# Performance work log

Measured on AMD Instinct MI355X. Metric: run time of the kernel, lower is better.

The kernel has to match this reference:

```python
import jax, jax.numpy as jnp
import numpy as np

RES = (32, 32, 32)   # S, H, W
WS = 4               # window size (cubic)
SHIFT = 2            # shift size
NH = 6               # num heads
C = 192              # dim
EPS = 1e-5


def _rel_pos_index(ws):
    coords = np.stack(np.meshgrid(np.arange(ws), np.arange(ws), np.arange(ws), indexing='ij'))
    cf = coords.reshape(3, -1)                      # (3, N)
    rc = (cf[:, :, None] - cf[:, None, :]).transpose(1, 2, 0).astype(np.int64)  # (N,N,3)
    rc[..., 0] += ws - 1
    rc[..., 1] += ws - 1
    rc[..., 2] += ws - 1
    rc[..., 0] *= 3 * ws - 1
    rc[..., 1] *= 2 * ws - 1
    return rc.sum(-1)                               # (N, N)

_RPI = jnp.asarray(_rel_pos_index(WS))


def _ln(x, g, b):
    m = jnp.mean(x, axis=-1, keepdims=True)
    v = jnp.mean(jnp.square(x - m), axis=-1, keepdims=True)
    return (x - m) * jax.lax.rsqrt(v + EPS) * g + b


def setup_inputs():
    key = jax.random.key(0)
    ks = jax.random.split(key, 12)
    B, L = 2, RES[0] * RES[1] * RES[2]
    nW, N = 512, WS ** 3
    Hd = 4 * C
    p = lambda k, s: jax.random.normal(k, s, jnp.float32) * 0.02
    return {
        'x': jax.random.normal(ks[0], (B, L, C), jnp.float32),
        'mask_matrix': jax.random.normal(ks[1], (nW, N, N), jnp.float32),
        'skip': jax.random.normal(ks[2], (B, L, C), jnp.float32),
        'x_up': jax.random.normal(ks[3], (B, L, C), jnp.float32),
        'norm1_g': jnp.ones((C,), jnp.float32), 'norm1_b': jnp.zeros((C,), jnp.float32),
        'kv_w': p(ks[4], (C, 2 * C)), 'kv_b': jnp.zeros((2 * C,), jnp.float32),
        'rpb_table': p(ks[5], ((2 * WS - 1) ** 3, NH)),
        'proj_w': p(ks[6], (C, C)), 'proj_b': jnp.zeros((C,), jnp.float32),
        'norm2_g': jnp.ones((C,), jnp.float32), 'norm2_b': jnp.zeros((C,), jnp.float32),
        'fc1_w': p(ks[7], (C, Hd)), 'fc1_b': jnp.zeros((Hd,), jnp.float32),
        'fc2_w': p(ks[8], (Hd, C)), 'fc2_b': jnp.zeros((C,), jnp.float32),
    }


def reference(x, mask_matrix, skip, x_up, norm1_g, norm1_b, kv_w, kv_b, rpb_table,
              proj_w, proj_b, norm2_g, norm2_b, fc1_w, fc1_b, fc2_w, fc2_b):
    B, L, _ = x.shape
    S, H, W = RES
    ws, N = WS, WS ** 3
    hd = C // NH
    scale = hd ** -0.5

    sn = _ln(skip, norm1_g, norm1_b).reshape(B, S, H, W, C)
    qn = _ln(x_up, norm1_g, norm1_b).reshape(B, S, H, W, C)
    # cyclic shift (shift_size > 0)
    sn = jnp.roll(sn, (-SHIFT, -SHIFT, -SHIFT), axis=(1, 2, 3))
    qn = jnp.roll(qn, (-SHIFT, -SHIFT, -SHIFT), axis=(1, 2, 3))

    def part(t):  # window partition -> (B*nW, N, C)
        t = t.reshape(B, S // ws, ws, H // ws, ws, W // ws, ws, C)
        return t.transpose(0, 1, 3, 5, 2, 4, 6, 7).reshape(-1, N, C)

    skw, qw = part(sn), part(qn)
    B_ = skw.shape[0]

    kv = (skw @ kv_w + kv_b).reshape(B_, N, 2, NH, hd)
    k = kv[:, :, 0].transpose(0, 2, 1, 3)   # (B_, NH, N, hd)
    v = kv[:, :, 1].transpose(0, 2, 1, 3)
    q = qw.reshape(B_, N, NH, hd).transpose(0, 2, 1, 3) * scale

    attn = jnp.einsum('bhqd,bhkd->bhqk', q, k)
    rpb = rpb_table[_RPI.reshape(-1)].reshape(N, N, NH).transpose(2, 0, 1)  # (NH, N, N)
    attn = attn + rpb[None]
    nW = mask_matrix.shape[0]
    attn = attn.reshape(B, nW, NH, N, N) + mask_matrix[None, :, None]
    attn = jax.nn.softmax(attn.reshape(B_, NH, N, N), axis=-1)

    out = jnp.einsum('bhqk,bhkd->bhqd', attn, v).transpose(0, 2, 1, 3).reshape(B_, N, C)
    out = out @ proj_w + proj_b

    # window reverse
    out = out.reshape(B, S // ws, H // ws, W // ws, ws, ws, ws, C)
    out = out.transpose(0, 1, 4, 2, 5, 3, 6, 7).reshape(B, S, H, W, C)
    out = jnp.roll(out, (SHIFT, SHIFT, SHIFT), axis=(1, 2, 3)).reshape(B, L, C)

    x = x + out
    h = _ln(x, norm2_g, norm2_b)
    h = jax.nn.gelu(h @ fc1_w + fc1_b, approximate=False) @ fc2_w + fc2_b
    return x + h
```

## Files before the change

### kernel.cpp

```cpp
#include <hip/hip_runtime.h>
#include <math.h>

typedef unsigned short u16;
typedef __bf16 bf16x8 __attribute__((ext_vector_type(8)));
typedef float f32x4 __attribute__((ext_vector_type(4)));
typedef unsigned short u16x8 __attribute__((ext_vector_type(8)));

#define SHIFT 2

static __device__ __forceinline__ f32x4 mfma16(bf16x8 a, bf16x8 b, f32x4 c) {
  return __builtin_amdgcn_mfma_f32_16x16x32_bf16(a, b, c, 0, 0, 0);
}
static __device__ __forceinline__ u16 f2bf(float f) {
  unsigned u = __builtin_bit_cast(unsigned, f);
  unsigned r = u + 0x7fffu + ((u >> 16) & 1u);
  return (u16)(r >> 16);
}
static __device__ __forceinline__ float bf2f(u16 u) {
  unsigned v = (unsigned)u << 16;
  return __builtin_bit_cast(float, v);
}
static __device__ __forceinline__ void stage16(const u16* g, u16* lbase, int lane) {
#if __has_builtin(__builtin_amdgcn_global_load_lds)
  __builtin_amdgcn_global_load_lds(
      (const __attribute__((address_space(1))) unsigned int*)g,
      (__attribute__((address_space(3))) unsigned int*)lbase, 16, 0, 0);
#else
  *(u16x8*)(lbase + lane * 8) = *(const u16x8*)g;
#endif
}

#define OFF_KVWT  ((size_t)0)
#define OFF_PRWT  (OFF_KVWT + 384*192*2)
#define OFF_FC1WT (OFF_PRWT + 192*192*2)
#define OFF_FC2WT (OFF_FC1WT + 768*192*2)
#define OFF_SKW   (OFF_FC2WT + 192*768*2)
#define OFF_QW    (OFF_SKW + (size_t)65536*192*2)
#define OFF_KVB   (OFF_QW + (size_t)65536*192*2)
#define OFF_POX   (OFF_KVB + (size_t)65536*384*2)
#define OFF_YB    (OFF_POX + (size_t)65536*192*2)
#define OFF_HN    (OFF_YB + (size_t)65536*192*2)
#define OFF_RPBG  (OFF_HN + (size_t)65536*192*2)

__global__ __launch_bounds__(256) void k_prep(
    const float* __restrict__ kv_w, const float* __restrict__ proj_w,
    const float* __restrict__ fc1_w, const float* __restrict__ fc2_w,
    const float* __restrict__ rpb,
    u16* __restrict__ kvT, u16* __restrict__ prT,
    u16* __restrict__ f1T, u16* __restrict__ f2T, u16* __restrict__ rpbg) {
  int i = blockIdx.x * 256 + threadIdx.x;
  if (i < 192 * 384) kvT[(i % 384) * 192 + i / 384] = f2bf(kv_w[i]);
  if (i < 192 * 192) prT[(i % 192) * 192 + i / 192] = f2bf(proj_w[i]);
  if (i < 192 * 768) f1T[(i % 768) * 192 + i / 768] = f2bf(fc1_w[i]);
  if (i < 768 * 192) f2T[(i % 192) * 768 + i / 192] = f2bf(fc2_w[i]);
  if (i < 24576) {
    int h = i >> 12, rem = i & 4095, qr = rem >> 6, kc = rem & 63;
    int qs = qr >> 4, qh = (qr >> 2) & 3, qx = qr & 3;
    int ks = kc >> 4, kh = (kc >> 2) & 3, kx = kc & 3;
    int idx = (qs - ks + 3) * 11 + (qh - kh + 3) * 7 + (qx - kx + 3);
    rpbg[i] = f2bf(rpb[idx * 6 + h]);
  }
}

__global__ __launch_bounds__(256) void k_ln_part(
    const float* __restrict__ skip, const float* __restrict__ x_up,
    const float* __restrict__ gam, const float* __restrict__ bet,
    u16* __restrict__ skw, u16* __restrict__ qw) {
  int row = blockIdx.x * 4 + (threadIdx.x >> 6);
  int lane = threadIdx.x & 63;
  const float* sp = skip + (size_t)row * 192;
  const float* qp = x_up + (size_t)row * 192;
  float sv[3], qv[3], ss = 0.f, qs = 0.f;
#pragma unroll
  for (int j = 0; j < 3; j++) {
    sv[j] = sp[lane + 64 * j]; qv[j] = qp[lane + 64 * j];
    ss += sv[j]; qs += qv[j];
  }
#pragma unroll
  for (int m = 1; m < 64; m <<= 1) { ss += __shfl_xor(ss, m, 64); qs += __shfl_xor(qs, m, 64); }
  float sm = ss * (1.f / 192.f), qm = qs * (1.f / 192.f);
  float s2 = 0.f, q2 = 0.f;
#pragma unroll
  for (int j = 0; j < 3; j++) { float d = sv[j] - sm; s2 += d * d; d = qv[j] - qm; q2 += d * d; }
#pragma unroll
  for (int m = 1; m < 64; m <<= 1) { s2 += __shfl_xor(s2, m, 64); q2 += __shfl_xor(q2, m, 64); }
  float sr = rsqrtf(s2 * (1.f / 192.f) + 1e-5f), qr = rsqrtf(q2 * (1.f / 192.f) + 1e-5f);
  int b = row >> 15, l = row & 32767;
  int s = l >> 10, h = (l >> 5) & 31, w = l & 31;
  int s_ = (s - SHIFT) & 31, h_ = (h - SHIFT) & 31, w_ = (w - SHIFT) & 31;
  int wIdx = ((s_ >> 2) * 8 + (h_ >> 2)) * 8 + (w_ >> 2);
  int n = ((s_ & 3) * 4 + (h_ & 3)) * 4 + (w_ & 3);
  size_t orow = ((size_t)(b * 512 + wIdx) * 64 + n) * 192;
  const float scale = 0.17677669529663687f;
#pragma unroll
  for (int j = 0; j < 3; j++) {
    int cc = lane + 64 * j;
    float gg = gam[cc], bb = bet[cc];
    skw[orow + cc] = f2bf((sv[j] - sm) * sr * gg + bb);
    qw[orow + cc]  = f2bf(((qv[j] - qm) * qr * gg + bb) * scale);
  }
}

__global__ __launch_bounds__(256, 2) void k_kv(
    const u16* __restrict__ A, const u16* __restrict__ BT,
    const float* __restrict__ bias, u16* __restrict__ outh) {
  __shared__ u16 lw[192 * 192];
  int mb = blockIdx.x, nb = blockIdx.y;
  int tid = threadIdx.x, l = tid & 63, wv = tid >> 6, g = l >> 4, c = l & 15;
  int wr = wv >> 1, wc = wv & 1;
#pragma unroll
  for (int i = 0; i < 18; i++) {
    int CI = i * 256 + tid;
    int row = CI / 24, ch = CI % 24;
    int sch = (ch & 24) | ((ch ^ row) & 7);
    stage16(BT + (size_t)(nb * 192 + row) * 192 + sch * 8, lw + (i * 256 + wv * 64) * 8, l);
  }
  __syncthreads();
  f32x4 acc[4][6] = {};
#pragma unroll
  for (int ks = 0; ks < 6; ks++) {
    bf16x8 a[4];
#pragma unroll
    for (int m = 0; m < 4; m++)
      a[m] = *(const bf16x8*)&A[(size_t)(mb * 128 + wr * 64 + m * 16 + c) * 192 + ks * 32 + g * 8];
#pragma unroll
    for (int n = 0; n < 6; n++) {
      int col = wc * 96 + n * 16 + c;
      int ch = ks * 4 + g;
      int chp = (ch & 24) | ((ch ^ col) & 7);
      bf16x8 b = *(const bf16x8*)&lw[col * 192 + chp * 8];
#pragma unroll
      for (int m = 0; m < 4; m++) acc[m][n] = mfma16(a[m], b, acc[m][n]);
    }
  }
#pragma unroll
  for (int n = 0; n < 6; n++)
#pragma unroll
    for (int m = 0; m < 4; m++) {
      int col = nb * 192 + wc * 96 + n * 16 + c;
      float bb = bias[col];
#pragma unroll
      for (int r = 0; r < 4; r++) {
        int row = mb * 128 + wr * 64 + m * 16 + g * 4 + r;
        outh[(size_t)row * 384 + col] = f2bf(acc[m][n][r] + bb);
      }
    }
}

__global__ __launch_bounds__(384) void k_attn_mega(
    const u16* __restrict__ qw, const u16* __restrict__ kvb,
    const u16* __restrict__ rpbg, const float* __restrict__ mask,
    const u16* __restrict__ prT, const float* __restrict__ proj_b,
    u16* __restrict__ pox) {
  __shared__ __align__(16) char smem[38400];
  u16* lv = (u16*)smem;
  u16* lo = (u16*)smem;
  u16* lp = (u16*)(smem + 24576);
  int b_ = blockIdx.x, wIdx = b_ & 511;
  int tid = threadIdx.x, l = tid & 63, wv = tid >> 6, g = l >> 4, c = l & 15;
  int h = wv;
#pragma unroll
  for (int i = 0; i < 4; i++) {
    int CI = i * 384 + tid;
    int row = CI / 24, ch = CI % 24;
    stage16(kvb + ((size_t)b_ * 64 + row) * 384 + 192 + ch * 8,
            lv + (i * 384 + wv * 64) * 8, l);
  }
  const float* mrow = mask + (size_t)wIdx * 4096;
  float4 mv[4][4];
#pragma unroll
  for (int n = 0; n < 4; n++)
#pragma unroll
    for (int m = 0; m < 4; m++)
      mv[n][m] = *(const float4*)&mrow[(n * 16 + c) * 64 + m * 16 + g * 4];
  bf16x8 qa[4], kb[4];
#pragma unroll
  for (int m = 0; m < 4; m++)
    qa[m] = *(const bf16x8*)&qw[((size_t)b_ * 64 + m * 16 + c) * 192 + h * 32 + g * 8];
#pragma unroll
  for (int n = 0; n < 4; n++)
    kb[n] = *(const bf16x8*)&kvb[((size_t)b_ * 64 + n * 16 + c) * 384 + h * 32 + g * 8];
  __syncthreads();
  bf16x8 vb[2][2];
#pragma unroll
  for (int kk = 0; kk < 2; kk++)
#pragma unroll
    for (int nd = 0; nd < 2; nd++) {
      union { u16 u[8]; bf16x8 v; } bb;
#pragma unroll
      for (int j = 0; j < 8; j++)
        bb.u[j] = lv[(kk * 32 + g * 8 + j) * 192 + h * 32 + nd * 16 + c];
      vb[kk][nd] = bb.v;
    }
  __syncthreads();
  f32x4 acc[4][4] = {};
#pragma unroll
  for (int m = 0; m < 4; m++)
#pragma unroll
    for (int n = 0; n < 4; n++) acc[m][n] = mfma16(kb[m], qa[n], acc[m][n]);
  const u16* rg = rpbg + h * 4096;
  f32x4 oacc[4][2] = {};
#pragma unroll
  for (int n = 0; n < 4; n++) {
    ushort4 rv[4];
#pragma unroll
    for (int m = 0; m < 4; m++)
      rv[m] = *(const ushort4*)&rg[(n * 16 + c) * 64 + m * 16 + g * 4];
    float vals[4][4];
    float mx = -3.4e38f;
#pragma unroll
    for (int m = 0; m < 4; m++) {
      float mr[4] = {mv[n][m].x, mv[n][m].y, mv[n][m].z, mv[n][m].w};
      u16 ru[4] = {rv[m].x, rv[m].y, rv[m].z, rv[m].w};
#pragma unroll
      for (int r = 0; r < 4; r++) {
        vals[m][r] = acc[m][n][r] + bf2f(ru[r]) + mr[r];
        mx = fmaxf(mx, vals[m][r]);
      }
    }
    mx = fmaxf(mx, __shfl_xor(mx, 16, 64));
    mx = fmaxf(mx, __shfl_xor(mx, 32, 64));
    float sum = 0.f;
#pragma unroll
    for (int m = 0; m < 4; m++)
#pragma unroll
      for (int r = 0; r < 4; r++) { vals[m][r] = __expf(vals[m][r] - mx); sum += vals[m][r]; }
    sum += __shfl_xor(sum, 16, 64);
    sum += __shfl_xor(sum, 32, 64);
    float inv = 1.f / sum;
#pragma unroll
    for (int m = 0; m < 4; m++) {
      unsigned p0 = f2bf(vals[m][0] * inv) | ((unsigned)f2bf(vals[m][1] * inv) << 16);
      unsigned p1 = f2bf(vals[m][2] * inv) | ((unsigned)f2bf(vals[m][3] * inv) << 16);
      *(uint2*)&lp[h * 1152 + c * 72 + m * 16 + g * 4] = make_uint2(p0, p1);
    }
#pragma unroll
    for (int kk = 0; kk < 2; kk++) {
      bf16x8 pa = *(const bf16x8*)&lp[h * 1152 + c * 72 + kk * 32 + g * 8];
#pragma unroll
      for (int nd = 0; nd < 2; nd++) oacc[n][nd] = mfma16(pa, vb[kk][nd], oacc[n][nd]);
    }
  }
  __syncthreads();
#pragma unroll
  for (int m = 0; m < 4; m++)
#pragma unroll
    for (int nd = 0; nd < 2; nd++)
#pragma unroll
      for (int r = 0; r < 4; r++)
        lo[(m * 16 + g * 4 + r) * 200 + h * 32 + nd * 16 + c] = f2bf(oacc[m][nd][r]);
  __syncthreads();
  f32x4 pacc[4][2] = {};
#pragma unroll
  for (int ks = 0; ks < 6; ks++) {
    bf16x8 pa[4];
#pragma unroll
    for (int m = 0; m < 4; m++)
      pa[m] = *(const bf16x8*)&lo[(m * 16 + c) * 200 + ks * 32 + g * 8];
#pragma unroll
    for (int n = 0; n < 2; n++) {
      bf16x8 pb = *(const bf16x8*)&prT[(size_t)(wv * 32 + n * 16 + c) * 192 + ks * 32 + g * 8];
#pragma unroll
      for (int m = 0; m < 4; m++) pacc[m][n] = mfma16(pa[m], pb, pacc[m][n]);
    }
  }
#pragma unroll
  for (int m = 0; m < 4; m++)
#pragma unroll
    for (int r = 0; r < 4; r++) {
      int tok = m * 16 + g * 4 + r;
#pragma unroll
      for (int n = 0; n < 2; n++) {
        int col = wv * 32 + n * 16 + c;
        pox[((size_t)b_ * 64 + tok) * 192 + col] = f2bf(pacc[m][n][r] + proj_b[col]);
      }
    }
}

__global__ __launch_bounds__(256) void k_ln2(
    const float* __restrict__ x, const u16* __restrict__ pox,
    const float* __restrict__ g2, const float* __restrict__ b2,
    u16* __restrict__ yb, u16* __restrict__ hn) {
  int row = blockIdx.x * 4 + (threadIdx.x >> 6);
  int lane = threadIdx.x & 63;
  int b = row >> 15, ll = row & 32767;
  int s = ll >> 10, hh = (ll >> 5) & 31, w = ll & 31;
  int s_ = (s - SHIFT) & 31, h_ = (hh - SHIFT) & 31, w_ = (w - SHIFT) & 31;
  int wI = ((s_ >> 2) * 8 + (h_ >> 2)) * 8 + (w_ >> 2);
  int n = ((s_ & 3) * 4 + (h_ & 3)) * 4 + (w_ & 3);
  size_t wrow = ((size_t)(b * 512 + wI) * 64 + n) * 192;
  float y[3]; float ss = 0.f, sq = 0.f;
#pragma unroll
  for (int j = 0; j < 3; j++) {
    int cc = lane + 64 * j;
    y[j] = x[(size_t)row * 192 + cc] + bf2f(pox[wrow + cc]);
    ss += y[j]; sq += y[j] * y[j];
  }
#pragma unroll
  for (int m = 1; m < 64; m <<= 1) { ss += __shfl_xor(ss, m, 64); sq += __shfl_xor(sq, m, 64); }
  float mu = ss * (1.f / 192.f);
  float rs = rsqrtf(sq * (1.f / 192.f) - mu * mu + 1e-5f);
#pragma unroll
  for (int j = 0; j < 3; j++) {
    int cc = lane + 64 * j;
    yb[(size_t)row * 192 + cc] = f2bf(y[j]);
    hn[(size_t)row * 192 + cc] = f2bf((y[j] - mu) * rs * g2[cc] + b2[cc]);
  }
}

__global__ __launch_bounds__(256) void k_mlp(
    const u16* __restrict__ hn, const u16* __restrict__ f1T,
    const u16* __restrict__ f2T, const float* __restrict__ b1,
    const float* __restrict__ b2f, const u16* __restrict__ yb,
    float* __restrict__ out) {
  __shared__ u16 lds[29184];
  u16* f1c = lds;
  u16* f2c = lds + 12288;
  u16* h1c = lds + 24576;
  int tid = threadIdx.x, l = tid & 63, wv = tid >> 6, g = l >> 4, c = l & 15;
  size_t tokbase = (size_t)blockIdx.x * 64;
#pragma unroll
  for (int i = 0; i < 6; i++) {
    int CI = i * 256 + wv * 64 + l;
    int row = CI / 24, chp = CI % 24;
    int sch = (chp & 24) | ((chp ^ row) & 7);
    stage16(hn + (tokbase + row) * 192 + sch * 8, f1c + (i * 256 + wv * 64) * 8, l);
  }
  __syncthreads();
  bf16x8 hb[4][6];
#pragma unroll
  for (int tf = 0; tf < 4; tf++)
#pragma unroll
    for (int ks = 0; ks < 6; ks++) {
      int ch = ks * 4 + g;
      int chp = (ch & 24) | ((ch ^ c) & 7);
      hb[tf][ks] = *(const bf16x8*)&f1c[(tf * 16 + c) * 192 + chp * 8];
    }
  f32x4 acc2[3][4] = {};
#pragma unroll 1
  for (int ko = 0; ko < 12; ko++) {
    __syncthreads();
#pragma unroll
    for (int i = 0; i < 6; i++) {
      int CI = i * 256 + wv * 64 + l;
      int row = CI / 24, chp = CI % 24;
      int sch = (chp & 24) | ((chp ^ row) & 7);
      stage16(f1T + (size_t)(ko * 64 + row) * 192 + sch * 8,
              f1c + (i * 256 + wv * 64) * 8, l);
    }
#pragma unroll
    for (int i = 0; i < 6; i++) {
      int CI = i * 256 + wv * 64 + l;
      int row = CI >> 3, chp = CI & 7;
      int sch = chp ^ (row & 7);
      stage16(f2T + (size_t)row * 768 + ko * 64 + sch * 8,
              f2c + (i * 256 + wv * 64) * 8, l);
    }
    __syncthreads();
    f32x4 acc1[4] = {};
#pragma unroll
    for (int ks = 0; ks < 6; ks++) {
      int ch = ks * 4 + g;
      int chp = (ch & 24) | ((ch ^ c) & 7);
      bf16x8 wa = *(const bf16x8*)&f1c[(wv * 16 + c) * 192 + chp * 8];
#pragma unroll
      for (int tf = 0; tf < 4; tf++) acc1[tf] = mfma16(wa, hb[tf][ks], acc1[tf]);
    }
    float4 b1v = *(const float4*)&b1[ko * 64 + wv * 16 + g * 4];
#pragma unroll
    for (int tf = 0; tf < 4; tf++) {
      unsigned pk[2];
#pragma unroll
      for (int p = 0; p < 2; p++) {
        unsigned lohi[2];
#pragma unroll
        for (int q = 0; q < 2; q++) {
          int r = p * 2 + q;
          float v = acc1[tf][r] + (r == 0 ? b1v.x : r == 1 ? b1v.y : r == 2 ? b1v.z : b1v.w);
          float u2 = v * (1.5957691216f + 0.0713548163f * v * v);
          v = v * (1.f / (1.f + __expf(-u2)));
          lohi[q] = f2bf(v);
        }
        pk[p] = lohi[0] | (lohi[1] << 16);
      }
      *(uint2*)&h1c[(tf * 16 + c) * 72 + wv * 16 + g * 4] = make_uint2(pk[0], pk[1]);
    }
    __syncthreads();
#pragma unroll
    for (int ck = 0; ck < 2; ck++) {
      bf16x8 a2[4];
#pragma unroll
      for (int tf = 0; tf < 4; tf++)
        a2[tf] = *(const bf16x8*)&h1c[(tf * 16 + c) * 72 + ck * 32 + g * 8];
#pragma unroll
      for (int of = 0; of < 3; of++) {
        int ch = ck * 4 + g;
        int chp = ch ^ (c & 7);
        bf16x8 wb = *(const bf16x8*)&f2c[(wv * 48 + of * 16 + c) * 64 + chp * 8];
#pragma unroll
        for (int tf = 0; tf < 4; tf++) acc2[of][tf] = mfma16(a2[tf], wb, acc2[of][tf]);
      }
    }
  }
#pragma unroll
  for (int of = 0; of < 3; of++)
#pragma unroll
    for (int tf = 0; tf < 4; tf++) {
      int col = wv * 48 + of * 16 + c;
      float bb = b2f[col];
#pragma unroll
      for (int r = 0; r < 4; r++) {
        size_t tok = tokbase + tf * 16 + g * 4 + r;
        size_t base = tok * 192 + col;
        out[base] = acc2[of][tf][r] + bb + bf2f(yb[base]);
      }
    }
}

extern "C" void kernel_launch(void* const* d_in, const int* in_sizes, int n_in,
                              void* d_out, int out_size, void* d_ws, size_t ws_size,
                              hipStream_t stream) {
  const float* x      = (const float*)d_in[0];
  const float* mask   = (const float*)d_in[1];
  const float* skip   = (const float*)d_in[2];
  const float* x_up   = (const float*)d_in[3];
  const float* n1g    = (const float*)d_in[4];
  const float* n1b    = (const float*)d_in[5];
  const float* kv_w   = (const float*)d_in[6];
  const float* kv_b   = (const float*)d_in[7];
  const float* rpb    = (const float*)d_in[8];
  const float* proj_w = (const float*)d_in[9];
  const float* proj_b = (const float*)d_in[10];
  const float* n2g    = (const float*)d_in[11];
  const float* n2b    = (const float*)d_in[12];
  const float* fc1_w  = (const float*)d_in[13];
  const float* fc1_b  = (const float*)d_in[14];
  const float* fc2_w  = (const float*)d_in[15];
  const float* fc2_b  = (const float*)d_in[16];
  char* ws = (char*)d_ws;
  u16* kvT  = (u16*)(ws + OFF_KVWT);
  u16* prT  = (u16*)(ws + OFF_PRWT);
  u16* f1T  = (u16*)(ws + OFF_FC1WT);
  u16* f2T  = (u16*)(ws + OFF_FC2WT);
  u16* skw  = (u16*)(ws + OFF_SKW);
  u16* qw   = (u16*)(ws + OFF_QW);
  u16* kvb  = (u16*)(ws + OFF_KVB);
  u16* pox  = (u16*)(ws + OFF_POX);
  u16* yb   = (u16*)(ws + OFF_YB);
  u16* hn   = (u16*)(ws + OFF_HN);
  u16* rpbg = (u16*)(ws + OFF_RPBG);
  float* out = (float*)d_out;

  k_prep<<<dim3(576), dim3(256), 0, stream>>>(kv_w, proj_w, fc1_w, fc2_w, rpb,
                                              kvT, prT, f1T, f2T, rpbg);
  k_ln_part<<<dim3(16384), dim3(256), 0, stream>>>(skip, x_up, n1g, n1b, skw, qw);
  k_kv<<<dim3(512, 2), dim3(256), 0, stream>>>(skw, kvT, kv_b, kvb);
  k_attn_mega<<<dim3(1024), dim3(384), 0, stream>>>(
      qw, kvb, rpbg, mask, prT, proj_b, pox);
  k_ln2<<<dim3(16384), dim3(256), 0, stream>>>(x, pox, n2g, n2b, yb, hn);
  k_mlp<<<dim3(1024), dim3(256), 0, stream>>>(
      hn, f1T, f2T, fc1_b, fc2_b, yb, out);
}
```

Baseline: 223.3 us.

## Repartition MLP kernel so each wave owns 16 tokens and prefetch weights early

The fused MLP kernel now has each wave own 16 tokens across all hidden and output columns, rather than splitting hidden and output columns across waves. Each wave loads its token activations straight from global into registers, and its GELU hidden tile stays in a private LDS region. The fc1 and fc2 weight chunks for the next iteration are staged right after the barrier that frees them, so loads overlap the other GEMM. This aims to cut barrier stalls and expose load latency, but costs more accumulator registers (12 output fragments) and more LDS weight reads per MFMA.

```diff
diff --git a/kernel.cpp b/kernel.cpp
--- a/kernel.cpp
+++ b/kernel.cpp
@@ -318,57 +318,44 @@
   u16* f2c = lds + 12288;
   u16* h1c = lds + 24576;
   int tid = threadIdx.x, l = tid & 63, wv = tid >> 6, g = l >> 4, c = l & 15;
-  size_t tokbase = (size_t)blockIdx.x * 64;
+  size_t tok0 = (size_t)blockIdx.x * 64 + wv * 16;
+  u16* tile = h1c + wv * 1152;
+  bf16x8 hb[6];
+#pragma unroll
+  for (int ks = 0; ks < 6; ks++)
+    hb[ks] = *(const bf16x8*)&hn[(tok0 + c) * 192 + ks * 32 + g * 8];
 #pragma unroll
   for (int i = 0; i < 6; i++) {
-    int CI = i * 256 + wv * 64 + l;
-    int row = CI / 24, chp = CI % 24;
-    int sch = (chp & 24) | ((chp ^ row) & 7);
-    stage16(hn + (tokbase + row) * 192 + sch * 8, f1c + (i * 256 + wv * 64) * 8, l);
-  }
-  __syncthreads();
-  bf16x8 hb[4][6];
-#pragma unroll
-  for (int tf = 0; tf < 4; tf++)
+    int CI = i * 256 + tid;
+    int row = CI / 24, chs = CI % 24;
+    int sch = (chs & 24) | ((chs ^ row) & 7);
+    stage16(f1T + (size_t)row * 192 + sch * 8, f1c + (i * 256 + wv * 64) * 8, l);
+  }
+#pragma unroll
+  for (int i = 0; i < 6; i++) {
+    int CI = i * 256 + tid;
+    int row = CI >> 3, chs = CI & 7;
+    int sch = chs ^ (row & 7);
+    stage16(f2T + (size_t)row * 768 + sch * 8, f2c + (i * 256 + wv * 64) * 8, l);
+  }
+  __syncthreads();
+  f32x4 acc2[12] = {};
+#pragma unroll 1
+  for (int ko = 0; ko < 12; ko++) {
+    f32x4 acc1[4] = {};
 #pragma unroll
     for (int ks = 0; ks < 6; ks++) {
       int ch = ks * 4 + g;
       int chp = (ch & 24) | ((ch ^ c) & 7);
-      hb[tf][ks] = *(const bf16x8*)&f1c[(tf * 16 + c) * 192 + chp * 8];
-    }
-  f32x4 acc2[3][4] = {};
-#pragma unroll 1
-  for (int ko = 0; ko < 12; ko++) {
-    __syncthreads();
-#pragma unroll
-    for (int i = 0; i < 6; i++) {
-      int CI = i * 256 + wv * 64 + l;
-      int row = CI / 24, chp = CI % 24;
-      int sch = (chp & 24) | ((chp ^ row) & 7);
-      stage16(f1T + (size_t)(ko * 64 + row) * 192 + sch * 8,
-              f1c + (i * 256 + wv * 64) * 8, l);
-    }
-#pragma unroll
-    for (int i = 0; i < 6; i++) {
-      int CI = i * 256 + wv * 64 + l;
-      int row = CI >> 3, chp = CI & 7;
-      int sch = chp ^ (row & 7);
-      stage16(f2T + (size_t)row * 768 + ko * 64 + sch * 8,
-              f2c + (i * 256 + wv * 64) * 8, l);
-    }
-    __syncthreads();
-    f32x4 acc1[4] = {};
-#pragma unroll
-    for (int ks = 0; ks < 6; ks++) {
-      int ch = ks * 4 + g;
-      int chp = (ch & 24) | ((ch ^ c) & 7);
-      bf16x8 wa = *(const bf16x8*)&f1c[(wv * 16 + c) * 192 + chp * 8];
-#pragma unroll
-      for (int tf = 0; tf < 4; tf++) acc1[tf] = mfma16(wa, hb[tf][ks], acc1[tf]);
-    }
-    float4 b1v = *(const float4*)&b1[ko * 64 + wv * 16 + g * 4];
-#pragma unroll
-    for (int tf = 0; tf < 4; tf++) {
+#pragma unroll
+      for (int cf = 0; cf < 4; cf++) {
+        bf16x8 wa = *(const bf16x8*)&f1c[(cf * 16 + c) * 192 + chp * 8];
+        acc1[cf] = mfma16(wa, hb[ks], acc1[cf]);
+      }
+    }
+#pragma unroll
+    for (int cf = 0; cf < 4; cf++) {
+      float4 b1v = *(const float4*)&b1[ko * 64 + cf * 16 + g * 4];
       unsigned pk[2];
 #pragma unroll
       for (int p = 0; p < 2; p++) {
@@ -376,45 +363,60 @@
 #pragma unroll
         for (int q = 0; q < 2; q++) {
           int r = p * 2 + q;
-          float v = acc1[tf][r] + (r == 0 ? b1v.x : r == 1 ? b1v.y : r == 2 ? b1v.z : b1v.w);
+          float v = acc1[cf][r] + (r == 0 ? b1v.x : r == 1 ? b1v.y : r == 2 ? b1v.z : b1v.w);
           float u2 = v * (1.5957691216f + 0.0713548163f * v * v);
           v = v * (1.f / (1.f + __expf(-u2)));
           lohi[q] = f2bf(v);
         }
         pk[p] = lohi[0] | (lohi[1] << 16);
       }
-      *(uint2*)&h1c[(tf * 16 + c) * 72 + wv * 16 + g * 4] = make_uint2(pk[0], pk[1]);
+      *(uint2*)&tile[c * 72 + cf * 16 + g * 4] = make_uint2(pk[0], pk[1]);
     }
     __syncthreads();
+    if (ko < 11) {
+#pragma unroll
+      for (int i = 0; i < 6; i++) {
+        int CI = i * 256 + tid;
+        int row = CI / 24, chs = CI % 24;
+        int sch = (chs & 24) | ((chs ^ row) & 7);
+        stage16(f1T + (size_t)((ko + 1) * 64 + row) * 192 + sch * 8,
+                f1c + (i * 256 + wv * 64) * 8, l);
+      }
+    }
 #pragma unroll
     for (int ck = 0; ck < 2; ck++) {
-      bf16x8 a2[4];
-#pragma unroll
-      for (int tf = 0; tf < 4; tf++)
-        a2[tf] = *(const bf16x8*)&h1c[(tf * 16 + c) * 72 + ck * 32 + g * 8];
-#pragma unroll
-      for (int of = 0; of < 3; of++) {
-        int ch = ck * 4 + g;
-        int chp = ch ^ (c & 7);
-        bf16x8 wb = *(const bf16x8*)&f2c[(wv * 48 + of * 16 + c) * 64 + chp * 8];
-#pragma unroll
-        for (int tf = 0; tf < 4; tf++) acc2[of][tf] = mfma16(a2[tf], wb, acc2[of][tf]);
-      }
-    }
-  }
-#pragma unroll
-  for (int of = 0; of < 3; of++)
-#pragma unroll
-    for (int tf = 0; tf < 4; tf++) {
-      int col = wv * 48 + of * 16 + c;
-      float bb = b2f[col];
-#pragma unroll
-      for (int r = 0; r < 4; r++) {
-        size_t tok = tokbase + tf * 16 + g * 4 + r;
-        size_t base = tok * 192 + col;
-        out[base] = acc2[of][tf][r] + bb + bf2f(yb[base]);
-      }
-    }
+      bf16x8 a2 = *(const bf16x8*)&tile[c * 72 + ck * 32 + g * 8];
+      int ch = ck * 4 + g;
+      int chp = ch ^ (c & 7);
+#pragma unroll
+      for (int of = 0; of < 12; of++) {
+        bf16x8 wb = *(const bf16x8*)&f2c[(of * 16 + c) * 64 + chp * 8];
+        acc2[of] = mfma16(a2, wb, acc2[of]);
+      }
+    }
+    __syncthreads();
+    if (ko < 11) {
+#pragma unroll
+      for (int i = 0; i < 6; i++) {
+        int CI = i * 256 + tid;
+        int row = CI >> 3, chs = CI & 7;
+        int sch = chs ^ (row & 7);
+        stage16(f2T + (size_t)row * 768 + (ko + 1) * 64 + sch * 8,
+                f2c + (i * 256 + wv * 64) * 8, l);
+      }
+    }
+  }
+#pragma unroll
+  for (int of = 0; of < 12; of++) {
+    int col = of * 16 + c;
+    float bb = b2f[col];
+#pragma unroll
+    for (int r = 0; r < 4; r++) {
+      size_t trow = tok0 + g * 4 + r;
+      size_t base = trow * 192 + col;
+      out[base] = acc2[of][r] + bb + bf2f(yb[base]);
+    }
+  }
 }
 
 extern "C" void kernel_launch(void* const* d_in, const int* in_sizes, int n_in,
```

Result: no change. 223.9 us (+0.3%).
